# Optimization experiments

Measured on AMD Instinct MI355X. Metric: run time of the kernel, lower is better.

## Reference

```python
import jax, jax.numpy as jnp
import numpy as np

DIM = 2048
INNER = 5632  # multiple_of*ceil((2*8192/3)/multiple_of) with multiple_of=256
E = 8
TOP_K = 2


def setup_inputs() -> dict:
    key = jax.random.key(0)
    ks = jax.random.split(key, 5)
    scale = 0.02
    hidden_states = jax.random.normal(ks[0], (2, 1024, DIM), dtype=jnp.float32)
    gate_w = jax.random.normal(ks[1], (E, DIM), dtype=jnp.float32) * scale   # torch Linear: [out,in]
    w1 = jax.random.normal(ks[2], (E, INNER, DIM), dtype=jnp.float32) * scale
    w2 = jax.random.normal(ks[3], (E, DIM, INNER), dtype=jnp.float32) * scale
    w3 = jax.random.normal(ks[4], (E, INNER, DIM), dtype=jnp.float32) * scale
    return {"hidden_states": hidden_states, "gate_w": gate_w, "w1": w1, "w2": w2, "w3": w3}


def reference(hidden_states, gate_w, w1, w2, w3):
    B, S, D = hidden_states.shape
    x = hidden_states.reshape(-1, D)                      # [T, D]
    T = x.shape[0]
    # router: softmax in float32, then top-k and renormalize
    router_logits = x @ gate_w.T                          # [T, E]
    probs = jax.nn.softmax(router_logits.astype(jnp.float32), axis=-1)
    routing_weights, selected = jax.lax.top_k(probs, TOP_K)  # [T, K]
    routing_weights = routing_weights / routing_weights.sum(-1, keepdims=True)
    # per-token weight for each expert (0 if not selected)
    expert_w = jnp.zeros((T, E), dtype=routing_weights.dtype)
    expert_w = expert_w.at[jnp.arange(T)[:, None], selected].add(routing_weights)  # [T, E]
    # dense SwiGLU FFN for every expert on every token (matches original loop)
    h = jax.nn.silu(jnp.einsum('td,ehd->eth', x, w1)) * jnp.einsum('td,ehd->eth', x, w3)  # [E,T,INNER]
    out = jnp.einsum('eth,edh->etd', h, w2)               # [E, T, D]
    final = jnp.einsum('etd,te->td', out, expert_w.astype(out.dtype))
    return final.reshape(B, S, D)
```

## Files before the change

### kernel.cpp

```cpp
#include <hip/hip_runtime.h>
#include <hip/hip_bf16.h>
#include <cstdint>
#include <cstddef>


#define TOKS  2048
#define DIMSZ 2048
#define INNER 5632
#define NEXP  8

typedef __attribute__((ext_vector_type(8))) short short8;
typedef __attribute__((ext_vector_type(4))) float f32x4;

__device__ __forceinline__ unsigned short f2bf(float f) {
  __hip_bfloat16 b = __float2bfloat16(f);
  return __builtin_bit_cast(unsigned short, b);
}

__device__ __forceinline__ short8 pack8(float4 a, float4 b) {
  short8 s;
  s[0] = (short)f2bf(a.x); s[1] = (short)f2bf(a.y);
  s[2] = (short)f2bf(a.z); s[3] = (short)f2bf(a.w);
  s[4] = (short)f2bf(b.x); s[5] = (short)f2bf(b.y);
  s[6] = (short)f2bf(b.z); s[7] = (short)f2bf(b.w);
  return s;
}

__device__ __forceinline__ void gload16(const unsigned short* src, short8* dst) {
  __builtin_amdgcn_global_load_lds(
      (const __attribute__((address_space(1))) void*)src,
      (__attribute__((address_space(3))) void*)dst, 16, 0, 0);
}

__global__ void __launch_bounds__(64)
router_kernel(const float* __restrict__ x, const float* __restrict__ gw,
              int* __restrict__ sel, float* __restrict__ wts) {
  const int t = blockIdx.x;
  const int l = threadIdx.x;
  const float* xr = x + (size_t)t * DIMSZ;
  float xv[32];
#pragma unroll
  for (int i = 0; i < 32; ++i) xv[i] = xr[l + 64 * i];
  float lg[NEXP];
#pragma unroll
  for (int e = 0; e < NEXP; ++e) {
    const float* gr = gw + e * DIMSZ;
    float s = 0.f;
#pragma unroll
    for (int i = 0; i < 32; ++i) s += xv[i] * gr[l + 64 * i];
#pragma unroll
    for (int off = 32; off > 0; off >>= 1) s += __shfl_down(s, off, 64);
    lg[e] = s;
  }
  if (l == 0) {
    float m = lg[0];
#pragma unroll
    for (int e = 1; e < NEXP; ++e) m = fmaxf(m, lg[e]);
    float p[NEXP];
#pragma unroll
    for (int e = 0; e < NEXP; ++e) p[e] = __expf(lg[e] - m);
    int i1 = 0;
#pragma unroll
    for (int e = 1; e < NEXP; ++e) if (p[e] > p[i1]) i1 = e;
    int i2 = (i1 == 0) ? 1 : 0;
#pragma unroll
    for (int e = 0; e < NEXP; ++e) if (e != i1 && p[e] > p[i2]) i2 = e;
    float den = p[i1] + p[i2];
    sel[2 * t] = i1; sel[2 * t + 1] = i2;
    wts[2 * t] = p[i1] / den; wts[2 * t + 1] = p[i2] / den;
  }
}

__global__ void __launch_bounds__(512)
compact_kernel(const int* __restrict__ sel, const float* __restrict__ wts,
               int* __restrict__ cnt, int* __restrict__ offs,
               int* __restrict__ tok, float* __restrict__ twt) {
  const int w = threadIdx.x >> 6;
  const int l = threadIdx.x & 63;
  int c = 0;
  for (int base = 0; base < 2 * TOKS; base += 64) {
    int s = base + l;
    bool m = (sel[s] == w);
    unsigned long long mask = __ballot(m);
    int pre = __popcll(mask & ((1ull << l) - 1ull));
    if (m) {
      tok[w * TOKS + c + pre] = s >> 1;
      twt[w * TOKS + c + pre] = wts[s];
    }
    c += __popcll(mask);
  }
  if (l == 0) cnt[w] = c;
  __syncthreads();
  if (threadIdx.x == 0) {
    int acc = 0;
    for (int e = 0; e < NEXP; ++e) { offs[e] = acc; acc += cnt[e]; }
  }
}

__global__ void __launch_bounds__(256)
cvtx_kernel(const float* __restrict__ x, unsigned short* __restrict__ xbf) {
  const int i = blockIdx.x * 256 + threadIdx.x;
  const float4* src = (const float4*)x;
  ((short8*)xbf)[i] = pack8(src[2 * i], src[2 * i + 1]);
}

__global__ void __launch_bounds__(256)
cvtw_kernel(const float* __restrict__ src, unsigned short* __restrict__ dst, int n8) {
  const int stride = gridDim.x * 256;
  for (int i = blockIdx.x * 256 + threadIdx.x; i < n8; i += stride) {
    const float4* s = (const float4*)src + 2 * (size_t)i;
    ((short8*)dst)[i] = pack8(s[0], s[1]);
  }
}

__global__ void __launch_bounds__(256, 3)
gemm1_bf(const unsigned short* __restrict__ xbf,
         const unsigned short* __restrict__ w1b, const unsigned short* __restrict__ w3b,
         const int* __restrict__ cnt, const int* __restrict__ offs,
         const int* __restrict__ tok, unsigned short* __restrict__ h) {
  const int NWG   = (INNER / 64) * NEXP * 16;
  const int CHUNK = NWG / 8;
  const int lid = (blockIdx.x & 7) * CHUNK + (blockIdx.x >> 3);
  const int my = lid & 15;
  const int e  = (lid >> 4) & 7;
  const int bx = lid >> 7;
  const int n_e = cnt[e];
  if (n_e == 0 || my * 128 >= n_e) return;
  const int n0 = bx * 64;
  const int tid = threadIdx.x;
  const int lane = tid & 63;
  const int wid = tid >> 6;
  const int wm = wid >> 1, wn = wid & 1;

  __shared__ short8 As[1024];
  __shared__ short8 B1s[512];
  __shared__ short8 B3s[512];

  const unsigned short* aptr[4];
#pragma unroll
  for (int i = 0; i < 4; ++i) {
    int sl = i * 256 + wid * 64 + lane;
    int row = sl >> 3, g = sl & 7;
    int ri = my * 128 + row; if (ri >= n_e) ri = n_e - 1;
    int tkn = tok[e * TOKS + ri];
    aptr[i] = xbf + (size_t)tkn * DIMSZ + ((g ^ (row & 7)) * 8);
  }
  const unsigned short* b1ptr[2]; const unsigned short* b3ptr[2];
#pragma unroll
  for (int i = 0; i < 2; ++i) {
    int sl = i * 256 + wid * 64 + lane;
    int row = sl >> 3, g = sl & 7;
    size_t off = (size_t)e * INNER * DIMSZ + (size_t)(n0 + row) * DIMSZ + (g ^ (row & 7)) * 8;
    b1ptr[i] = w1b + off;
    b3ptr[i] = w3b + off;
  }

  f32x4 acc1[4][2] = {};
  f32x4 acc3[4][2] = {};

  for (int k0 = 0; k0 < DIMSZ; k0 += 64) {
#pragma unroll
    for (int i = 0; i < 4; ++i) gload16(aptr[i] + k0, &As[i * 256 + wid * 64]);
#pragma unroll
    for (int i = 0; i < 2; ++i) {
      gload16(b1ptr[i] + k0, &B1s[i * 256 + wid * 64]);
      gload16(b3ptr[i] + k0, &B3s[i * 256 + wid * 64]);
    }
    __syncthreads();
#pragma unroll
    for (int ks = 0; ks < 2; ++ks) {
      const int kg = ks * 4 + (lane >> 4);
      short8 af[4], b1f[2], b3f[2];
#pragma unroll
      for (int m = 0; m < 4; ++m) {
        int row = wm * 64 + m * 16 + (lane & 15);
        af[m] = As[row * 8 + (kg ^ (row & 7))];
      }
#pragma unroll
      for (int n = 0; n < 2; ++n) {
        int row = wn * 32 + n * 16 + (lane & 15);
        int idx = row * 8 + (kg ^ (row & 7));
        b1f[n] = B1s[idx];
        b3f[n] = B3s[idx];
      }
#pragma unroll
      for (int m = 0; m < 4; ++m)
#pragma unroll
        for (int n = 0; n < 2; ++n) {
          acc1[m][n] = __builtin_amdgcn_mfma_f32_16x16x32_bf16(af[m], b1f[n], acc1[m][n], 0, 0, 0);
          acc3[m][n] = __builtin_amdgcn_mfma_f32_16x16x32_bf16(af[m], b3f[n], acc3[m][n], 0, 0, 0);
        }
    }
    __syncthreads();
  }

  const int obase = offs[e];
#pragma unroll
  for (int m = 0; m < 4; ++m)
#pragma unroll
    for (int r = 0; r < 4; ++r) {
      int i = my * 128 + wm * 64 + m * 16 + (lane >> 4) * 4 + r;
      if (i < n_e) {
        unsigned short* hp = h + (size_t)(obase + i) * INNER + n0 + wn * 32 + (lane & 15);
#pragma unroll
        for (int n = 0; n < 2; ++n) {
          float v1 = acc1[m][n][r];
          float v3 = acc3[m][n][r];
          float hv = __fdividef(v1, 1.f + __expf(-v1)) * v3;
          hp[n * 16] = f2bf(hv);
        }
      }
    }
}

__global__ void __launch_bounds__(256, 3)
gemm2_bf(const unsigned short* __restrict__ h, const unsigned short* __restrict__ w2b,
         const int* __restrict__ cnt, const int* __restrict__ offs,
         const int* __restrict__ tok, const float* __restrict__ twt,
         float* __restrict__ out) {
  const int NWG   = (DIMSZ / 128) * NEXP * 16;
  const int CHUNK = NWG / 8;
  const int lid = (blockIdx.x & 7) * CHUNK + (blockIdx.x >> 3);
  const int my = lid & 15;
  const int e  = (lid >> 4) & 7;
  const int bx = lid >> 7;
  const int n_e = cnt[e];
  if (n_e == 0 || my * 128 >= n_e) return;
  const int n0 = bx * 128;
  const int tid = threadIdx.x;
  const int lane = tid & 63;
  const int wid = tid >> 6;
  const int wm = wid >> 1, wn = wid & 1;
  const int obase = offs[e];

  __shared__ short8 As[1024];
  __shared__ short8 Bs[1024];

  const unsigned short* aptr[4];
#pragma unroll
  for (int i = 0; i < 4; ++i) {
    int sl = i * 256 + wid * 64 + lane;
    int row = sl >> 3, g = sl & 7;
    int ri = my * 128 + row; if (ri >= n_e) ri = n_e - 1;
    aptr[i] = h + (size_t)(obase + ri) * INNER + ((g ^ (row & 7)) * 8);
  }
  const unsigned short* bptr[4];
#pragma unroll
  for (int i = 0; i < 4; ++i) {
    int sl = i * 256 + wid * 64 + lane;
    int row = sl >> 3, g = sl & 7;
    bptr[i] = w2b + (size_t)e * DIMSZ * INNER + (size_t)(n0 + row) * INNER + (g ^ (row & 7)) * 8;
  }

  f32x4 acc[4][4] = {};

  for (int k0 = 0; k0 < INNER; k0 += 64) {
#pragma unroll
    for (int i = 0; i < 4; ++i) {
      gload16(aptr[i] + k0, &As[i * 256 + wid * 64]);
      gload16(bptr[i] + k0, &Bs[i * 256 + wid * 64]);
    }
    __syncthreads();
#pragma unroll
    for (int ks = 0; ks < 2; ++ks) {
      const int kg = ks * 4 + (lane >> 4);
      short8 af[4], bf[4];
#pragma unroll
      for (int m = 0; m < 4; ++m) {
        int row = wm * 64 + m * 16 + (lane & 15);
        af[m] = As[row * 8 + (kg ^ (row & 7))];
      }
#pragma unroll
      for (int n = 0; n < 4; ++n) {
        int row = wn * 64 + n * 16 + (lane & 15);
        bf[n] = Bs[row * 8 + (kg ^ (row & 7))];
      }
#pragma unroll
      for (int m = 0; m < 4; ++m)
#pragma unroll
        for (int n = 0; n < 4; ++n)
          acc[m][n] = __builtin_amdgcn_mfma_f32_16x16x32_bf16(af[m], bf[n], acc[m][n], 0, 0, 0);
    }
    __syncthreads();
  }

#pragma unroll
  for (int m = 0; m < 4; ++m)
#pragma unroll
    for (int r = 0; r < 4; ++r) {
      int i = my * 128 + wm * 64 + m * 16 + (lane >> 4) * 4 + r;
      if (i < n_e) {
        int t = tok[e * TOKS + i];
        float wt = twt[e * TOKS + i];
        float* op = out + (size_t)t * DIMSZ + n0 + wn * 64 + (lane & 15);
#pragma unroll
        for (int n = 0; n < 4; ++n)
          atomicAdd(op + n * 16, acc[m][n][r] * wt);
      }
    }
}

__global__ void __launch_bounds__(256, 2)
gemm1_f32(const unsigned short* __restrict__ xbf,
          const float* __restrict__ w1, const float* __restrict__ w3,
          const int* __restrict__ cnt, const int* __restrict__ offs,
          const int* __restrict__ tok, unsigned short* __restrict__ h) {
  const int e = blockIdx.z;
  const int n_e = cnt[e];
  const int by = blockIdx.y;
  if (n_e == 0 || by * 128 >= n_e) return;
  const int n0 = blockIdx.x * 128;
  const int tid = threadIdx.x;
  const int lane = tid & 63;
  const int wid = tid >> 6;
  const int wm = wid >> 1, wn = wid & 1;

  __shared__ short8 As[1024];
  __shared__ short8 B1s[1024];
  __shared__ short8 B3s[1024];

  const unsigned short* asrc[4];
  int adst[4];
#pragma unroll
  for (int rep = 0; rep < 4; ++rep) {
    int flat = rep * 256 + tid;
    int row = flat >> 3, g = flat & 7;
    int ri = by * 128 + row;
    if (ri >= n_e) ri = n_e - 1;
    int tkn = tok[e * TOKS + ri];
    asrc[rep] = xbf + (size_t)tkn * DIMSZ + g * 8;
    adst[rep] = row * 8 + (g ^ (row & 7));
  }
  const float* w1e = w1 + (size_t)e * INNER * DIMSZ;
  const float* w3e = w3 + (size_t)e * INNER * DIMSZ;
  const float* b1src[2]; const float* b3src[2];
  int bd0[2], bd1[2];
#pragma unroll
  for (int rep = 0; rep < 2; ++rep) {
    int row = rep * 64 + (tid >> 2);
    int gb = (tid & 3) * 2;
    b1src[rep] = w1e + (size_t)(n0 + row) * DIMSZ + gb * 8;
    b3src[rep] = w3e + (size_t)(n0 + row) * DIMSZ + gb * 8;
    bd0[rep] = row * 8 + (gb ^ (row & 7));
    bd1[rep] = row * 8 + ((gb + 1) ^ (row & 7));
  }

  f32x4 acc1[4][4] = {};
  f32x4 acc3[4][4] = {};

#pragma unroll 1
  for (int k0 = 0; k0 < DIMSZ; k0 += 64) {
#pragma unroll
    for (int rep = 0; rep < 4; ++rep)
      As[adst[rep]] = *(const short8*)(asrc[rep] + k0);
#pragma unroll
    for (int rep = 0; rep < 2; ++rep) {
      const float4* p = (const float4*)(b1src[rep] + k0);
      float4 a0 = p[0], a1 = p[1], a2 = p[2], a3 = p[3];
      B1s[bd0[rep]] = pack8(a0, a1);
      B1s[bd1[rep]] = pack8(a2, a3);
      const float4* q = (const float4*)(b3src[rep] + k0);
      float4 c0 = q[0], c1 = q[1], c2 = q[2], c3 = q[3];
      B3s[bd0[rep]] = pack8(c0, c1);
      B3s[bd1[rep]] = pack8(c2, c3);
    }
    __syncthreads();
#pragma unroll
    for (int ks = 0; ks < 2; ++ks) {
      const int kg = ks * 4 + (lane >> 4);
      short8 af[4], b1f[4], b3f[4];
#pragma unroll
      for (int m = 0; m < 4; ++m) {
        int row = wm * 64 + m * 16 + (lane & 15);
        af[m] = As[row * 8 + (kg ^ (row & 7))];
      }
#pragma unroll
      for (int n = 0; n < 4; ++n) {
        int row = wn * 64 + n * 16 + (lane & 15);
        int idx = row * 8 + (kg ^ (row & 7));
        b1f[n] = B1s[idx];
        b3f[n] = B3s[idx];
      }
#pragma unroll
      for (int m = 0; m < 4; ++m)
#pragma unroll
        for (int n = 0; n < 4; ++n) {
          acc1[m][n] = __builtin_amdgcn_mfma_f32_16x16x32_bf16(af[m], b1f[n], acc1[m][n], 0, 0, 0);
          acc3[m][n] = __builtin_amdgcn_mfma_f32_16x16x32_bf16(af[m], b3f[n], acc3[m][n], 0, 0, 0);
        }
    }
    __syncthreads();
  }

  const int obase = offs[e];
#pragma unroll
  for (int m = 0; m < 4; ++m)
#pragma unroll
    for (int r = 0; r < 4; ++r) {
      int i = by * 128 + wm * 64 + m * 16 + (lane >> 4) * 4 + r;
      if (i < n_e) {
        unsigned short* hp = h + (size_t)(obase + i) * INNER + n0 + wn * 64 + (lane & 15);
#pragma unroll
        for (int n = 0; n < 4; ++n) {
          float v1 = acc1[m][n][r];
          float v3 = acc3[m][n][r];
          float hv = __fdividef(v1, 1.f + __expf(-v1)) * v3;
          hp[n * 16] = f2bf(hv);
        }
      }
    }
}

__global__ void __launch_bounds__(256, 2)
gemm2_f32(const unsigned short* __restrict__ h, const float* __restrict__ w2,
          const int* __restrict__ cnt, const int* __restrict__ offs,
          const int* __restrict__ tok, const float* __restrict__ twt,
          float* __restrict__ out) {
  const int e = blockIdx.z;
  const int n_e = cnt[e];
  const int by = blockIdx.y;
  if (n_e == 0 || by * 128 >= n_e) return;
  const int n0 = blockIdx.x * 128;
  const int tid = threadIdx.x;
  const int lane = tid & 63;
  const int wid = tid >> 6;
  const int wm = wid >> 1, wn = wid & 1;
  const int obase = offs[e];

  __shared__ short8 As[1024];
  __shared__ short8 Bs[1024];

  const unsigned short* asrc[4];
  int adst[4];
#pragma unroll
  for (int rep = 0; rep < 4; ++rep) {
    int flat = rep * 256 + tid;
    int row = flat >> 3, g = flat & 7;
    int ri = by * 128 + row;
    if (ri >= n_e) ri = n_e - 1;
    asrc[rep] = h + (size_t)(obase + ri) * INNER + g * 8;
    adst[rep] = row * 8 + (g ^ (row & 7));
  }
  const float* w2e = w2 + (size_t)e * DIMSZ * INNER;
  const float* bsrc[2];
  int bd0[2], bd1[2];
#pragma unroll
  for (int rep = 0; rep < 2; ++rep) {
    int row = rep * 64 + (tid >> 2);
    int gb = (tid & 3) * 2;
    bsrc[rep] = w2e + (size_t)(n0 + row) * INNER + gb * 8;
    bd0[rep] = row * 8 + (gb ^ (row & 7));
    bd1[rep] = row * 8 + ((gb + 1) ^ (row & 7));
  }

  f32x4 acc[4][4] = {};

#pragma unroll 1
  for (int k0 = 0; k0 < INNER; k0 += 64) {
#pragma unroll
    for (int rep = 0; rep < 4; ++rep)
      As[adst[rep]] = *(const short8*)(asrc[rep] + k0);
#pragma unroll
    for (int rep = 0; rep < 2; ++rep) {
      const float4* p = (const float4*)(bsrc[rep] + k0);
      float4 a0 = p[0], a1 = p[1], a2 = p[2], a3 = p[3];
      Bs[bd0[rep]] = pack8(a0, a1);
      Bs[bd1[rep]] = pack8(a2, a3);
    }
    __syncthreads();
#pragma unroll
    for (int ks = 0; ks < 2; ++ks) {
      const int kg = ks * 4 + (lane >> 4);
      short8 af[4], bf[4];
#pragma unroll
      for (int m = 0; m < 4; ++m) {
        int row = wm * 64 + m * 16 + (lane & 15);
        af[m] = As[row * 8 + (kg ^ (row & 7))];
      }
#pragma unroll
      for (int n = 0; n < 4; ++n) {
        int row = wn * 64 + n * 16 + (lane & 15);
        bf[n] = Bs[row * 8 + (kg ^ (row & 7))];
      }
#pragma unroll
      for (int m = 0; m < 4; ++m)
#pragma unroll
        for (int n = 0; n < 4; ++n)
          acc[m][n] = __builtin_amdgcn_mfma_f32_16x16x32_bf16(af[m], bf[n], acc[m][n], 0, 0, 0);
    }
    __syncthreads();
  }

#pragma unroll
  for (int m = 0; m < 4; ++m)
#pragma unroll
    for (int r = 0; r < 4; ++r) {
      int i = by * 128 + wm * 64 + m * 16 + (lane >> 4) * 4 + r;
      if (i < n_e) {
        int t = tok[e * TOKS + i];
        float wt = twt[e * TOKS + i];
        float* op = out + (size_t)t * DIMSZ + n0 + wn * 64 + (lane & 15);
#pragma unroll
        for (int n = 0; n < 4; ++n)
          atomicAdd(op + n * 16, acc[m][n][r] * wt);
      }
    }
}

extern "C" void kernel_launch(void* const* d_in, const int* in_sizes, int n_in,
                              void* d_out, int out_size, void* d_ws, size_t ws_size,
                              hipStream_t stream) {
  (void)in_sizes; (void)n_in;
  const float* x  = (const float*)d_in[0];
  const float* gw = (const float*)d_in[1];
  const float* w1 = (const float*)d_in[2];
  const float* w2 = (const float*)d_in[3];
  const float* w3 = (const float*)d_in[4];
  float* out = (float*)d_out;

  char* ws = (char*)d_ws;
  int*            sel  = (int*)(ws);
  float*          wts  = (float*)(ws + (16 << 10));
  int*            cnt  = (int*)(ws + (32 << 10));
  int*            offs = (int*)(ws + (32 << 10) + 64);
  int*            tok  = (int*)(ws + (33 << 10));
  float*          twt  = (float*)(ws + (97 << 10));
  unsigned short* xbf  = (unsigned short*)(ws + (1 << 20));
  unsigned short* h    = (unsigned short*)(ws + (16 << 20));

  const size_t WELEM = (size_t)NEXP * INNER * DIMSZ;
  const size_t WB    = WELEM * 2;
  unsigned short* w1bf = (unsigned short*)(ws + (64ull << 20));
  unsigned short* w3bf = (unsigned short*)(ws + (64ull << 20) + WB);
  const size_t NEED = (64ull << 20) + 2 * WB;

  hipMemsetAsync(out, 0, (size_t)out_size * sizeof(float), stream);
  cvtx_kernel<<<2048, 256, 0, stream>>>(x, xbf);
  router_kernel<<<TOKS, 64, 0, stream>>>(x, gw, sel, wts);
  compact_kernel<<<1, 512, 0, stream>>>(sel, wts, cnt, offs, tok, twt);

  if (ws_size >= NEED) {
    const int n8 = (int)(WELEM / 8);
    cvtw_kernel<<<4096, 256, 0, stream>>>(w1, w1bf, n8);
    cvtw_kernel<<<4096, 256, 0, stream>>>(w3, w3bf, n8);
    gemm1_bf<<<(INNER / 64) * 16 * NEXP, 256, 0, stream>>>(
        xbf, w1bf, w3bf, cnt, offs, tok, h);
    cvtw_kernel<<<4096, 256, 0, stream>>>(w2, w1bf, n8);
    gemm2_bf<<<(DIMSZ / 128) * 16 * NEXP, 256, 0, stream>>>(
        h, w1bf, cnt, offs, tok, twt, out);
  } else {
    gemm1_f32<<<dim3(INNER / 128, TOKS / 128, NEXP), 256, 0, stream>>>(
        xbf, w1, w3, cnt, offs, tok, h);
    gemm2_f32<<<dim3(DIMSZ / 128, TOKS / 128, NEXP), 256, 0, stream>>>(
        h, w2, cnt, offs, tok, twt, out);
  }
}
```

Before: 862.5 us.

## Fuse fp32 W1/W3 conversion into gemm1 and overlap W2 conversion

Gemm1 now loads fp32 W1/W3 tiles straight into LDS and converts them to bf16 while building MFMA fragments, which drops the two separate weight-conversion passes and their bf16 writes and rereads. The W2 conversion moves into extra trailing blocks of the same launch so it can run alongside the GEMM blocks. In exchange, gemm1 reads twice as many weight bytes per tile, uses more LDS (which may lower occupancy), and does per-fragment conversion work, with each weight tile reread by up to 16 token-tile blocks.

```diff
diff --git a/kernel.cpp b/kernel.cpp
--- a/kernel.cpp
+++ b/kernel.cpp
@@ -27,6 +27,11 @@
 }
 
 __device__ __forceinline__ void gload16(const unsigned short* src, short8* dst) {
+  __builtin_amdgcn_global_load_lds(
+      (const __attribute__((address_space(1))) void*)src,
+      (__attribute__((address_space(3))) void*)dst, 16, 0, 0);
+}
+__device__ __forceinline__ void gload16f(const float* src, float4* dst) {
   __builtin_amdgcn_global_load_lds(
       (const __attribute__((address_space(1))) void*)src,
       (__attribute__((address_space(3))) void*)dst, 16, 0, 0);
@@ -104,21 +109,25 @@
   ((short8*)xbf)[i] = pack8(src[2 * i], src[2 * i + 1]);
 }
 
-__global__ void __launch_bounds__(256)
-cvtw_kernel(const float* __restrict__ src, unsigned short* __restrict__ dst, int n8) {
-  const int stride = gridDim.x * 256;
-  for (int i = blockIdx.x * 256 + threadIdx.x; i < n8; i += stride) {
-    const float4* s = (const float4*)src + 2 * (size_t)i;
-    ((short8*)dst)[i] = pack8(s[0], s[1]);
-  }
-}
-
 __global__ void __launch_bounds__(256, 3)
-gemm1_bf(const unsigned short* __restrict__ xbf,
-         const unsigned short* __restrict__ w1b, const unsigned short* __restrict__ w3b,
+gemm1_fw(const unsigned short* __restrict__ xbf,
+         const float* __restrict__ w1, const float* __restrict__ w3,
+         const float* __restrict__ w2, unsigned short* __restrict__ w2bf,
          const int* __restrict__ cnt, const int* __restrict__ offs,
          const int* __restrict__ tok, unsigned short* __restrict__ h) {
   const int NWG   = (INNER / 64) * NEXP * 16;
+  const int tid = threadIdx.x;
+
+  if ((int)blockIdx.x >= NWG) {
+    const int b = blockIdx.x - NWG;
+    const int n8 = (int)(((size_t)NEXP * DIMSZ * INNER) / 8);
+    for (int i = b * 256 + tid; i < n8; i += 2048 * 256) {
+      const float4* s = (const float4*)w2 + 2 * (size_t)i;
+      ((short8*)w2bf)[i] = pack8(s[0], s[1]);
+    }
+    return;
+  }
+
   const int CHUNK = NWG / 8;
   const int lid = (blockIdx.x & 7) * CHUNK + (blockIdx.x >> 3);
   const int my = lid & 15;
@@ -127,14 +136,13 @@
   const int n_e = cnt[e];
   if (n_e == 0 || my * 128 >= n_e) return;
   const int n0 = bx * 64;
-  const int tid = threadIdx.x;
   const int lane = tid & 63;
   const int wid = tid >> 6;
   const int wm = wid >> 1, wn = wid & 1;
 
   __shared__ short8 As[1024];
-  __shared__ short8 B1s[512];
-  __shared__ short8 B3s[512];
+  __shared__ float4 B1s[1024];
+  __shared__ float4 B3s[1024];
 
   const unsigned short* aptr[4];
 #pragma unroll
@@ -145,14 +153,15 @@
     int tkn = tok[e * TOKS + ri];
     aptr[i] = xbf + (size_t)tkn * DIMSZ + ((g ^ (row & 7)) * 8);
   }
-  const unsigned short* b1ptr[2]; const unsigned short* b3ptr[2];
-#pragma unroll
-  for (int i = 0; i < 2; ++i) {
+  const float* b1p[4]; const float* b3p[4];
+#pragma unroll
+  for (int i = 0; i < 4; ++i) {
     int sl = i * 256 + wid * 64 + lane;
-    int row = sl >> 3, g = sl & 7;
-    size_t off = (size_t)e * INNER * DIMSZ + (size_t)(n0 + row) * DIMSZ + (g ^ (row & 7)) * 8;
-    b1ptr[i] = w1b + off;
-    b3ptr[i] = w3b + off;
+    int row = sl >> 4, gg = sl & 15;
+    size_t off = (size_t)e * INNER * DIMSZ + (size_t)(n0 + row) * DIMSZ
+               + ((gg ^ (row & 15)) * 4);
+    b1p[i] = w1 + off;
+    b3p[i] = w3 + off;
   }
 
   f32x4 acc1[4][2] = {};
@@ -162,9 +171,9 @@
 #pragma unroll
     for (int i = 0; i < 4; ++i) gload16(aptr[i] + k0, &As[i * 256 + wid * 64]);
 #pragma unroll
-    for (int i = 0; i < 2; ++i) {
-      gload16(b1ptr[i] + k0, &B1s[i * 256 + wid * 64]);
-      gload16(b3ptr[i] + k0, &B3s[i * 256 + wid * 64]);
+    for (int i = 0; i < 4; ++i) {
+      gload16f(b1p[i] + k0, &B1s[i * 256 + wid * 64]);
+      gload16f(b3p[i] + k0, &B3s[i * 256 + wid * 64]);
     }
     __syncthreads();
 #pragma unroll
@@ -179,9 +188,14 @@
 #pragma unroll
       for (int n = 0; n < 2; ++n) {
         int row = wn * 32 + n * 16 + (lane & 15);
-        int idx = row * 8 + (kg ^ (row & 7));
-        b1f[n] = B1s[idx];
-        b3f[n] = B3s[idx];
+        int base = row * 16;
+        int sw = row & 15;
+        float4 u0 = B1s[base + ((2 * kg) ^ sw)];
+        float4 u1 = B1s[base + ((2 * kg + 1) ^ sw)];
+        b1f[n] = pack8(u0, u1);
+        float4 v0 = B3s[base + ((2 * kg) ^ sw)];
+        float4 v1 = B3s[base + ((2 * kg + 1) ^ sw)];
+        b3f[n] = pack8(v0, v1);
       }
 #pragma unroll
       for (int m = 0; m < 4; ++m)
@@ -528,11 +542,9 @@
   unsigned short* xbf  = (unsigned short*)(ws + (1 << 20));
   unsigned short* h    = (unsigned short*)(ws + (16 << 20));
 
-  const size_t WELEM = (size_t)NEXP * INNER * DIMSZ;
-  const size_t WB    = WELEM * 2;
-  unsigned short* w1bf = (unsigned short*)(ws + (64ull << 20));
-  unsigned short* w3bf = (unsigned short*)(ws + (64ull << 20) + WB);
-  const size_t NEED = (64ull << 20) + 2 * WB;
+  const size_t WB = (size_t)NEXP * INNER * DIMSZ * 2;
+  unsigned short* w2bf = (unsigned short*)(ws + (64ull << 20));
+  const size_t NEED = (64ull << 20) + WB;
 
   hipMemsetAsync(out, 0, (size_t)out_size * sizeof(float), stream);
   cvtx_kernel<<<2048, 256, 0, stream>>>(x, xbf);
@@ -540,14 +552,10 @@
   compact_kernel<<<1, 512, 0, stream>>>(sel, wts, cnt, offs, tok, twt);
 
   if (ws_size >= NEED) {
-    const int n8 = (int)(WELEM / 8);
-    cvtw_kernel<<<4096, 256, 0, stream>>>(w1, w1bf, n8);
-    cvtw_kernel<<<4096, 256, 0, stream>>>(w3, w3bf, n8);
-    gemm1_bf<<<(INNER / 64) * 16 * NEXP, 256, 0, stream>>>(
-        xbf, w1bf, w3bf, cnt, offs, tok, h);
-    cvtw_kernel<<<4096, 256, 0, stream>>>(w2, w1bf, n8);
+    gemm1_fw<<<(INNER / 64) * 16 * NEXP + 2048, 256, 0, stream>>>(
+        xbf, w1, w3, w2, w2bf, cnt, offs, tok, h);
     gemm2_bf<<<(DIMSZ / 128) * 16 * NEXP, 256, 0, stream>>>(
-        h, w1bf, cnt, offs, tok, twt, out);
+        h, w2bf, cnt, offs, tok, twt, out);
   } else {
     gemm1_f32<<<dim3(INNER / 128, TOKS / 128, NEXP), 256, 0, stream>>>(
         xbf, w1, w3, cnt, offs, tok, h);
```

Measured after the change: 759.7 us. 1.14x faster.
